# Performance work log

Measured on AMD Instinct MI355X. Metric: run time of the kernel, lower is better.

The kernel has to match this reference:

```python
import math
import jax, jax.numpy as jnp
import numpy as np

H = 1024
NH = 16
HD = H // NH
FF = 4096


def gelu_erf(x):
    return x * 0.5 * (1.0 + jax.lax.erf(x / jnp.sqrt(jnp.float32(2.0))))


def layernorm(x, gamma, beta, eps=1e-12):
    mean = x.mean(axis=-1, keepdims=True)
    var = ((x - mean) ** 2).mean(axis=-1, keepdims=True)
    return gamma * (x - mean) / jnp.sqrt(var + eps) + beta


def setup_inputs() -> dict:
    key = jax.random.key(0)
    ks = jax.random.split(key, 12)
    B, S = 2, 2048
    sc = 0.02
    return {
        "x": jax.random.normal(ks[0], (B, S, H), jnp.float32),
        "attention_mask": jnp.ones((B, S), jnp.int32),
        "Wq": jax.random.normal(ks[1], (H, H), jnp.float32) * sc,
        "bq": jnp.zeros((H,), jnp.float32),
        "Wk": jax.random.normal(ks[2], (H, H), jnp.float32) * sc,
        "bk": jnp.zeros((H,), jnp.float32),
        "Wv": jax.random.normal(ks[3], (H, H), jnp.float32) * sc,
        "bv": jnp.zeros((H,), jnp.float32),
        "Wo": jax.random.normal(ks[4], (H, H), jnp.float32) * sc,
        "bo": jnp.zeros((H,), jnp.float32),
        "ln1_g": jnp.ones((H,), jnp.float32),
        "ln1_b": jnp.zeros((H,), jnp.float32),
        "W1": jax.random.normal(ks[5], (H, FF), jnp.float32) * sc,
        "b1": jnp.zeros((FF,), jnp.float32),
        "W2": jax.random.normal(ks[6], (FF, H), jnp.float32) * sc,
        "b2": jnp.zeros((H,), jnp.float32),
        "ln2_g": jnp.ones((H,), jnp.float32),
        "ln2_b": jnp.zeros((H,), jnp.float32),
    }


def reference(x, attention_mask, Wq, bq, Wk, bk, Wv, bv, Wo, bo,
              ln1_g, ln1_b, W1, b1, W2, b2, ln2_g, ln2_b):
    B, S, _ = x.shape
    # QKV projections, split heads -> [B, NH, S, HD]
    def split(t):
        return t.reshape(B, S, NH, HD).transpose(0, 2, 1, 3)
    q = split(x @ Wq + bq)
    k = split(x @ Wk + bk)
    v = split(x @ Wv + bv)
    # scores [B, NH, S, S]
    s = jnp.einsum("bhqd,bhkd->bhqk", q, k) / math.sqrt(HD)
    mask = (attention_mask == 1)[:, None, None, :]  # [B,1,1,S]
    s = jnp.where(mask, s, -jnp.inf)
    p = jax.nn.softmax(s, axis=-1)
    a = jnp.einsum("bhqk,bhkd->bhqd", p, v)
    a = a.transpose(0, 2, 1, 3).reshape(B, S, H)  # merge heads
    a = a @ Wo + bo
    a = layernorm(a, ln1_g, ln1_b)  # NOTE: no residual in source
    m = gelu_erf(a @ W1 + b1) @ W2 + b2
    return layernorm(m, ln2_g, ln2_b)
```

## Files before the change

### kernel.cpp

```cpp
#include <hip/hip_runtime.h>
#include <hip/hip_bf16.h>
#include <math.h>

typedef __bf16 bf16;
typedef __attribute__((ext_vector_type(8))) __bf16 bf16x8;
typedef __attribute__((ext_vector_type(4))) __bf16 bf16x4;
typedef __attribute__((ext_vector_type(2))) __bf16 bf16x2;
typedef __attribute__((ext_vector_type(4))) float f32x4;
typedef __attribute__((ext_vector_type(4))) short short4v;

#define HDIM 1024
#define NHEAD 16
#define HD 64
#define FFDIM 4096
#define BATCH 2
#define SEQ 2048
#define M_TOK 4096
#define NSPLIT 4
#define PSTRIDE ((size_t)M_TOK * HDIM)

static __device__ __forceinline__ void async_load16(const bf16* g, bf16* l) {
  __builtin_amdgcn_global_load_lds(
      (const __attribute__((address_space(1))) void*)g,
      (__attribute__((address_space(3))) void*)l, 16, 0, 0);
}

static __device__ __forceinline__ f32x4 mfma16_bf16(bf16x4 a, bf16x4 b, f32x4 c) {
#if defined(__HIP_DEVICE_COMPILE__)
#if __has_builtin(__builtin_amdgcn_mfma_f32_16x16x16bf16_1k)
  return __builtin_amdgcn_mfma_f32_16x16x16bf16_1k(
      __builtin_bit_cast(short4v, a), __builtin_bit_cast(short4v, b), c, 0, 0, 0);
#else
  return __builtin_amdgcn_mfma_f32_16x16x16_bf16(a, b, c, 0, 0, 0);
#endif
#else
  return c;
#endif
}

static __device__ __forceinline__ float gelu_erf_f(float x) {
  const float z = x * 0.70710678118f;
  const float az = fabsf(z);
  const float tt = __builtin_amdgcn_rcpf(fmaf(az, 0.3275911f, 1.0f));
  const float poly = tt * fmaf(tt, fmaf(tt, fmaf(tt, fmaf(tt, 1.061405429f,
                     -1.453152027f), 1.421413741f), -0.284496736f), 0.254829592f);
  const float e = __builtin_amdgcn_exp2f(az * az * -1.4426950408889634f);
  float erfv = 1.0f - poly * e;
  erfv = (z < 0.f) ? -erfv : erfv;
  return 0.5f * x * (1.0f + erfv);
}

__global__ __launch_bounds__(256)
void prep_kernel(const float* __restrict__ x,
                 const float* __restrict__ Wq, const float* __restrict__ Wk,
                 const float* __restrict__ Wv, const float* __restrict__ Wo,
                 const float* __restrict__ W1, const float* __restrict__ W2,
                 bf16* __restrict__ Xb, bf16* __restrict__ QKVT,
                 bf16* __restrict__ W1T, bf16* __restrict__ W2T)
{
  const int z = blockIdx.z;
  const int t = threadIdx.x;
  if (z == 12) {
    const size_t base = ((size_t)(blockIdx.y * 32 + blockIdx.x)) * 4096;
#pragma unroll
    for (int j = 0; j < 4; ++j) {
      const size_t i = base + j * 1024 + t * 4;
      f32x4 v = *(const f32x4*)(x + i);
      bf16x4 o;
#pragma unroll
      for (int k = 0; k < 4; ++k) o[k] = (bf16)v[k];
      *(bf16x4*)(Xb + i) = o;
    }
    return;
  }
  const float* ps; bf16* pd; int sld, dld;
  if (z < 4) {
    ps = (z == 0) ? Wq : (z == 1) ? Wk : (z == 2) ? Wv : Wo;
    pd = QKVT + (size_t)z * HDIM * HDIM; sld = 1024; dld = 1024;
  } else if (z < 8) {
    const int c = z - 4;
    ps = W1 + c * 1024; sld = 4096;
    pd = W1T + (size_t)c * 1024 * 1024; dld = 1024;
  } else {
    const int c = z - 8;
    ps = W2 + (size_t)c * 1024 * 1024; sld = 1024;
    pd = W2T + c * 1024; dld = 4096;
  }
  __shared__ float tile[32][33];
  const int tx = t & 31, ty = t >> 5;
  const int c0 = blockIdx.x * 32, r0 = blockIdx.y * 32;
#pragma unroll
  for (int i = 0; i < 32; i += 8)
    tile[ty + i][tx] = ps[(size_t)(r0 + ty + i) * sld + c0 + tx];
  __syncthreads();
  const int rr0 = (t & 15) * 2;
  const int ccb = t >> 4;
#pragma unroll
  for (int i = 0; i < 2; ++i) {
    const int cc = ccb + 16 * i;
    bf16x2 v = {(bf16)tile[rr0][cc], (bf16)tile[rr0 + 1][cc]};
    *(bf16x2*)(pd + (size_t)(c0 + cc) * dld + r0 + rr0) = v;
  }
}

#define BSW(R, C) ((R) * 64 + ((C) ^ (((R) & 7) << 3)))
#define BSW128(R, C) ((R) * 128 + ((C) ^ (((R) & 7) << 3)))

template<int EPI>
__global__ __launch_bounds__(256)
void gemm_bt(const bf16* __restrict__ A, const bf16* __restrict__ Bt,
             const float* __restrict__ b0, const float* __restrict__ b1p,
             const float* __restrict__ b2p, void* __restrict__ Cout,
             int M, int N, int ldk, int kchunk)
{
  __shared__ __align__(16) bf16 Smem[2][128 * 64];
  bf16* As = Smem[0];
  bf16* Bs = Smem[1];
  const int t = threadIdx.x;
  const int wave = t >> 6, lane = t & 63;
  const int lm = lane & 15, qd = lane >> 4;
  const int wm = (wave >> 1) * 64, wn = (wave & 1) * 64;

  const int nwg2d = gridDim.x * gridDim.y;
  const int cpx = nwg2d >> 3;
  const int lin2d = blockIdx.x + gridDim.x * blockIdx.y;
  const int swz = (lin2d & 7) * cpx + (lin2d >> 3);
  const int bxs = swz % gridDim.x;
  const int bys = swz / gridDim.x;
  const int bm = bys * 128, bn = bxs * 128;
  const int kbeg = blockIdx.z * kchunk;

  f32x4 acc[4][4] = {};
  const int srow = t >> 3;
  const int schk = t & 7;

  for (int k0 = kbeg; k0 < kbeg + kchunk; k0 += 64) {
#pragma unroll
    for (int r = 0; r < 4; ++r) {
      const int row = r * 32 + srow;
      const int chunk = schk ^ (row & 7);
      async_load16(A + (size_t)(bm + row) * ldk + (k0 + chunk * 8),
                   (bf16*)((char*)As + r * 4096 + t * 16));
    }
#pragma unroll
    for (int r = 0; r < 4; ++r) {
      const int row = r * 32 + srow;
      const int chunk = schk ^ (row & 7);
      async_load16(Bt + (size_t)(bn + row) * ldk + (k0 + chunk * 8),
                   (bf16*)((char*)Bs + r * 4096 + t * 16));
    }
    __syncthreads();
#pragma unroll
    for (int ks = 0; ks < 2; ++ks) {
      bf16x8 av[4], bv[4];
#pragma unroll
      for (int mt = 0; mt < 4; ++mt) {
        const int row = wm + mt * 16 + lm;
        const int chunk = (ks * 4 + qd) ^ (row & 7);
        av[mt] = *(const bf16x8*)(As + row * 64 + chunk * 8);
      }
#pragma unroll
      for (int nt = 0; nt < 4; ++nt) {
        const int row = wn + nt * 16 + lm;
        const int chunk = (ks * 4 + qd) ^ (row & 7);
        bv[nt] = *(const bf16x8*)(Bs + row * 64 + chunk * 8);
      }
#pragma unroll
      for (int mt = 0; mt < 4; ++mt)
#pragma unroll
        for (int nt = 0; nt < 4; ++nt)
          acc[mt][nt] = __builtin_amdgcn_mfma_f32_16x16x32_bf16(bv[nt], av[mt], acc[mt][nt], 0, 0, 0);
    }
    __syncthreads();
  }

  bf16* tw = &Smem[0][0] + wave * 4096;
  const bool vt = (EPI == 3) && ((bn + wn) >= 2 * HDIM);

#pragma unroll
  for (int nt = 0; nt < 4; ++nt) {
    const int n0 = bn + wn + nt * 16 + qd * 4;
    f32x4 bsv = {0.f, 0.f, 0.f, 0.f};
    if (EPI == 2) bsv = *(const f32x4*)(b0 + n0);
    if (EPI == 3) {
      const int sect = n0 >> 10, c = n0 & 1023;
      const float* bp = (sect == 0) ? b0 : (sect == 1) ? b1p : b2p;
      bsv = *(const f32x4*)(bp + c);
    }
#pragma unroll
    for (int mt = 0; mt < 4; ++mt) {
      f32x4 v;
#pragma unroll
      for (int r = 0; r < 4; ++r) v[r] = acc[mt][nt][r] + bsv[r];
      bf16x4 o;
      if (EPI == 2) {
#pragma unroll
        for (int r = 0; r < 4; ++r) o[r] = (bf16)gelu_erf_f(v[r]);
      } else {
#pragma unroll
        for (int r = 0; r < 4; ++r) o[r] = (bf16)v[r];
      }
      if (!vt) {
        *(bf16x4*)(tw + BSW(mt * 16 + lm, nt * 16 + qd * 4)) = o;
      } else {
#pragma unroll
        for (int r = 0; r < 4; ++r)
          tw[BSW(nt * 16 + qd * 4 + r, mt * 16 + lm)] = o[r];
      }
    }
  }
  const int erow = lane >> 3, ech = lane & 7;
  if (EPI == 1) {
    bf16* dst = (bf16*)Cout + (size_t)blockIdx.z * M * N +
                (size_t)(bm + wm) * N + (bn + wn);
#pragma unroll
    for (int p = 0; p < 8; ++p) {
      const int row = p * 8 + erow;
      bf16x8 val = *(const bf16x8*)(tw + BSW(row, ech * 8));
      *(bf16x8*)(dst + (size_t)row * N + ech * 8) = val;
    }
  } else if (EPI == 2) {
    bf16* dst = (bf16*)Cout + (size_t)(bm + wm) * N + (bn + wn);
#pragma unroll
    for (int p = 0; p < 8; ++p) {
      const int row = p * 8 + erow;
      bf16x8 val = *(const bf16x8*)(tw + BSW(row, ech * 8));
      *(bf16x8*)(dst + (size_t)row * N + ech * 8) = val;
    }
  } else {
    bf16* base = (bf16*)Cout;
    const int sect = (bn + wn) >> 10;
    if (!vt) {
      bf16* dst = base + (size_t)sect * M_TOK * HDIM +
                  (size_t)(bm + wm) * HDIM + ((bn + wn) & 1023);
#pragma unroll
      for (int p = 0; p < 8; ++p) {
        const int row = p * 8 + erow;
        bf16x8 val = *(const bf16x8*)(tw + BSW(row, ech * 8));
        *(bf16x8*)(dst + (size_t)row * HDIM + ech * 8) = val;
      }
    } else {
      const int c0 = (bn + wn) & 1023;
      const int hh = c0 >> 6;
      const int bb = (bm + wm) >> 11, ss0 = (bm + wm) & 2047;
      bf16* dst = base + (size_t)2 * M_TOK * HDIM +
                  (size_t)((bb * NHEAD + hh) * HD) * SEQ + ss0;
#pragma unroll
      for (int p = 0; p < 8; ++p) {
        const int row = p * 8 + erow;
        bf16x8 val = *(const bf16x8*)(tw + BSW(row, ech * 8));
        *(bf16x8*)(dst + (size_t)row * SEQ + ech * 8) = val;
      }
    }
  }
}


#define STAGE_Q(OP, BASEMN, LDSB, KOFF, Q) do { \
    const int rr_ = (Q) * 64 + (t >> 3); \
    const int gc_ = (t & 7) ^ (rr_ & 7); \
    async_load16((OP) + (size_t)((BASEMN) + rr_) * ldk + (KOFF) + gc_ * 8, \
                 (LDSB) + (Q) * 4096 + t * 8); \
  } while (0)

#define STAGE_HALF(OP, BASEMN, LDSB, KOFF, H) do { \
    STAGE_Q(OP, BASEMN, LDSB, KOFF, 2 * (H)); \
    STAGE_Q(OP, BASEMN, LDSB, KOFF, 2 * (H) + 1); \
  } while (0)

#define LOAD_AV(BUF, MH) do { \
    _Pragma("unroll") \
    for (int mt_ = 0; mt_ < 4; ++mt_) { \
      const int row_ = wm + (MH) * 64 + mt_ * 16 + lm; \
      _Pragma("unroll") \
      for (int ks_ = 0; ks_ < 2; ++ks_) { \
        const int c_ = (ks_ * 4 + qd) ^ (row_ & 7); \
        av[mt_][ks_] = *(const bf16x8*)(As_[BUF] + row_ * 64 + c_ * 8); \
      } \
    } \
  } while (0)

#define LOAD_BV(DST, BUF, NH) do { \
    _Pragma("unroll") \
    for (int nt_ = 0; nt_ < 2; ++nt_) { \
      const int row_ = wnb + (NH) * 32 + nt_ * 16 + lm; \
      _Pragma("unroll") \
      for (int ks_ = 0; ks_ < 2; ++ks_) { \
        const int c_ = (ks_ * 4 + qd) ^ (row_ & 7); \
        DST[nt_][ks_] = *(const bf16x8*)(Bs_[BUF] + row_ * 64 + c_ * 8); \
      } \
    } \
  } while (0)

#define MFMA_Q(MH, BV, NH) do { \
    __builtin_amdgcn_s_setprio(1); \
    _Pragma("unroll") \
    for (int mt_ = 0; mt_ < 4; ++mt_) \
      _Pragma("unroll") \
      for (int nt_ = 0; nt_ < 2; ++nt_) \
        _Pragma("unroll") \
        for (int ks_ = 0; ks_ < 2; ++ks_) \
          acc[(MH) * 4 + mt_][(NH) * 2 + nt_] = \
              __builtin_amdgcn_mfma_f32_16x16x32_bf16( \
                  BV[nt_][ks_], av[mt_][ks_], \
                  acc[(MH) * 4 + mt_][(NH) * 2 + nt_], 0, 0, 0); \
    __builtin_amdgcn_s_setprio(0); \
  } while (0)

#define SYNC_PRE() do { \
    __builtin_amdgcn_s_barrier(); \
    asm volatile("s_waitcnt lgkmcnt(0)" ::: "memory"); \
    __builtin_amdgcn_sched_barrier(0); \
  } while (0)
#define SYNC_POST() do { \
    __builtin_amdgcn_s_barrier(); \
    __builtin_amdgcn_sched_barrier(0); \
  } while (0)

#define VMCNT4() asm volatile("s_waitcnt vmcnt(4)" ::: "memory")

#define FOURPH(RB, WAB, KTA, WBB, KTB) do { \
     \
    LOAD_AV(RB, 0); LOAD_BV(bv0, RB, 0); \
    STAGE_HALF(A, bm, As_[WAB], kbeg + (KTA) * 64, 0); \
    SYNC_PRE(); MFMA_Q(0, bv0, 0); SYNC_POST(); \
     \
    LOAD_BV(bv1, RB, 1); \
    STAGE_HALF(A, bm, As_[WAB], kbeg + (KTA) * 64, 1); \
    SYNC_PRE(); MFMA_Q(0, bv1, 1); SYNC_POST(); \
     \
    LOAD_AV(RB, 1); \
    STAGE_HALF(Bt, bn, Bs_[WBB], kbeg + (KTB) * 64, 0); \
    SYNC_PRE(); MFMA_Q(1, bv0, 0); SYNC_POST(); \
     \
    STAGE_HALF(Bt, bn, Bs_[WBB], kbeg + (KTB) * 64, 1); \
    SYNC_PRE(); MFMA_Q(1, bv1, 1); VMCNT4(); SYNC_POST(); \
  } while (0)

template<int EPI>
__global__ __launch_bounds__(512, 2)
void gemm256(const bf16* __restrict__ A, const bf16* __restrict__ Bt,
             const float* __restrict__ b0, const float* __restrict__ b1p,
             const float* __restrict__ b2p, void* __restrict__ Cout,
             int M, int N, int ldk, int kchunk)
{
  __shared__ __align__(16) bf16 SmemAll[4][256 * 64];
  bf16* const As_[2] = {SmemAll[0], SmemAll[1]};
  bf16* const Bs_[2] = {SmemAll[2], SmemAll[3]};

  const int t = threadIdx.x;
  const int wave = t >> 6, lane = t & 63;
  const int lm = lane & 15, qd = lane >> 4;
  const int wm = (wave >> 2) * 128;
  const int wnb = (wave & 3) * 64;

  const int nwg2d = gridDim.x * gridDim.y;
  const int cpx = nwg2d >> 3;
  const int lin2d = blockIdx.x + gridDim.x * blockIdx.y;
  const int swz = (lin2d & 7) * cpx + (lin2d >> 3);
  const int bm = (swz / gridDim.x) * 256, bn = (swz % gridDim.x) * 256;
  const int kbeg = blockIdx.z * kchunk;
  const int NT = kchunk >> 6;

  f32x4 acc[8][4] = {};
  bf16x8 av[4][2], bv0[2][2], bv1[2][2];

  STAGE_HALF(Bt, bn, Bs_[0], kbeg, 0);
  STAGE_HALF(Bt, bn, Bs_[0], kbeg, 1);
  STAGE_HALF(A,  bm, As_[0], kbeg, 0);
  STAGE_HALF(A,  bm, As_[0], kbeg, 1);
  STAGE_HALF(Bt, bn, Bs_[1], kbeg + 64, 0);
  STAGE_HALF(Bt, bn, Bs_[1], kbeg + 64, 1);
  VMCNT4();
  SYNC_POST();

  for (int it = 0; it < NT / 2; ++it) {
    const int tb = 2 * it + 1;
    const int tc = (2 * it + 2) & (NT - 1);
    const int td = (2 * it + 3) & (NT - 1);
    FOURPH(0, 1, tb, 0, tc);
    FOURPH(1, 0, tc, 1, td);
  }

  bf16* tw = &SmemAll[0][0] + wave * 8192;
  const bool vt = (EPI == 3) && ((bn + wnb) >= 2 * HDIM);

#pragma unroll
  for (int nt4 = 0; nt4 < 4; ++nt4) {
    const int n0 = bn + wnb + nt4 * 16 + qd * 4;
    f32x4 bsv = {0.f, 0.f, 0.f, 0.f};
    if (EPI == 2) bsv = *(const f32x4*)(b0 + n0);
    if (EPI == 3) {
      const int sect = n0 >> 10, c = n0 & 1023;
      const float* bp = (sect == 0) ? b0 : (sect == 1) ? b1p : b2p;
      bsv = *(const f32x4*)(bp + c);
    }
#pragma unroll
    for (int mt8 = 0; mt8 < 8; ++mt8) {
      f32x4 v;
#pragma unroll
      for (int r = 0; r < 4; ++r) v[r] = acc[mt8][nt4][r] + bsv[r];
      bf16x4 o;
      if (EPI == 2) {
#pragma unroll
        for (int r = 0; r < 4; ++r) o[r] = (bf16)gelu_erf_f(v[r]);
      } else {
#pragma unroll
        for (int r = 0; r < 4; ++r) o[r] = (bf16)v[r];
      }
      if (!vt) {
        *(bf16x4*)(tw + BSW(mt8 * 16 + lm, nt4 * 16 + qd * 4)) = o;
      } else {
#pragma unroll
        for (int r = 0; r < 4; ++r)
          tw[BSW128(nt4 * 16 + qd * 4 + r, mt8 * 16 + lm)] = o[r];
      }
    }
  }
  const int erow = lane >> 3, ech = lane & 7;
  if (EPI != 3) {
    bf16* dst = (bf16*)Cout +
                ((EPI == 1) ? (size_t)blockIdx.z * M * N : (size_t)0) +
                (size_t)(bm + wm) * N + (bn + wnb);
#pragma unroll
    for (int p = 0; p < 16; ++p) {
      const int row = p * 8 + erow;
      bf16x8 val = *(const bf16x8*)(tw + BSW(row, ech * 8));
      *(bf16x8*)(dst + (size_t)row * N + ech * 8) = val;
    }
  } else {
    bf16* base = (bf16*)Cout;
    const int sect = (bn + wnb) >> 10;
    const int c0 = (bn + wnb) & 1023;
    if (!vt) {
      bf16* dst = base + (size_t)sect * M_TOK * HDIM +
                  (size_t)(bm + wm) * HDIM + c0;
#pragma unroll
      for (int p = 0; p < 16; ++p) {
        const int row = p * 8 + erow;
        bf16x8 val = *(const bf16x8*)(tw + BSW(row, ech * 8));
        *(bf16x8*)(dst + (size_t)row * HDIM + ech * 8) = val;
      }
    } else {
      const int hh = c0 >> 6;
      const int bb = (bm + wm) >> 11, ss0 = (bm + wm) & 2047;
      bf16* dst = base + (size_t)2 * M_TOK * HDIM +
                  (size_t)((bb * NHEAD + hh) * HD) * SEQ + ss0;
#pragma unroll
      for (int p = 0; p < 16; ++p) {
        const int row = p * 4 + qd;
        const int cc = lm * 8;
        bf16x8 val = *(const bf16x8*)(tw + BSW128(row, cc));
        *(bf16x8*)(dst + (size_t)row * SEQ + cc) = val;
      }
    }
  }
}

__global__ __launch_bounds__(256)
void attn_kernel(const bf16* __restrict__ Q, const bf16* __restrict__ Kg,
                 const bf16* __restrict__ Vt, const int* __restrict__ mask,
                 bf16* __restrict__ Po, float* __restrict__ Lp)
{
  __shared__ __align__(16) bf16 Ks[64 * 64];
  __shared__ __align__(16) bf16 Vs[64 * 64];
  __shared__ float madd[64];

  const int t = threadIdx.x;
  const int wave = t >> 6, lane = t & 63;
  const int lm = lane & 15, qd = lane >> 4;

  const int lin = blockIdx.x;
  const int g = (lin & 7) * 16 + (lin >> 7);
  const int qblk = (lin >> 3) & 15;
  const int bh = g >> 2;
  const int split = g & 3;
  const int b = bh >> 4, h = bh & 15;
  const int q0 = qblk * 128 + wave * 32;
  const int kv_beg = split * (SEQ / NSPLIT);

  bf16x8 qf[2][2];
#pragma unroll
  for (int qt = 0; qt < 2; ++qt)
#pragma unroll
    for (int ks = 0; ks < 2; ++ks)
      qf[qt][ks] = *(const bf16x8*)(Q + (size_t)(b * SEQ + q0 + qt * 16 + lm) * HDIM +
                                    h * HD + ks * 32 + qd * 8);

  const bf16 onev = (bf16)1.0f;
  const bf16x4 ones = {onev, onev, onev, onev};
  f32x4 lacc[2] = {};
  f32x4 oacc[2][4] = {};

  const int srow = t >> 3, schk = t & 7;
  const float C = 0.1803368801f;

  for (int kv0 = kv_beg; kv0 < kv_beg + SEQ / NSPLIT; kv0 += 64) {
#pragma unroll
    for (int r = 0; r < 2; ++r) {
      const int row = r * 32 + srow;
      const int g2 = schk ^ (row & 7);
      async_load16(Kg + (size_t)(b * SEQ + kv0 + row) * HDIM + h * HD + g2 * 8,
                   (bf16*)((char*)Ks + r * 4096 + t * 16));
      async_load16(Vt + (size_t)(bh * HD + row) * SEQ + kv0 + g2 * 8,
                   (bf16*)((char*)Vs + r * 4096 + t * 16));
    }
    if (t < 64) madd[t] = (mask[b * SEQ + kv0 + t] == 1) ? 0.f : -1.0e30f;
    __syncthreads();

    bf16x8 kf[2][4];
#pragma unroll
    for (int ks = 0; ks < 2; ++ks)
#pragma unroll
      for (int nt = 0; nt < 4; ++nt) {
        const int row = nt * 16 + lm;
        const int c = (ks * 4 + qd) ^ (row & 7);
        kf[ks][nt] = *(const bf16x8*)(Ks + row * 64 + c * 8);
      }

    bf16x4 pf[2][4];
#pragma unroll
    for (int qt = 0; qt < 2; ++qt) {
      f32x4 sacc[4] = {};
#pragma unroll
      for (int ks = 0; ks < 2; ++ks)
#pragma unroll
        for (int nt = 0; nt < 4; ++nt)
          sacc[nt] = __builtin_amdgcn_mfma_f32_16x16x32_bf16(kf[ks][nt], qf[qt][ks], sacc[nt], 0, 0, 0);
#pragma unroll
      for (int nt = 0; nt < 4; ++nt) {
        f32x4 ma = *(const f32x4*)(madd + nt * 16 + qd * 4);
#pragma unroll
        for (int r = 0; r < 4; ++r)
          pf[qt][nt][r] = (bf16)__builtin_amdgcn_exp2f(fmaf(sacc[nt][r], C, ma[r]));
        lacc[qt] = mfma16_bf16(ones, pf[qt][nt], lacc[qt]);
      }
    }

#pragma unroll
    for (int nt2 = 0; nt2 < 4; ++nt2) {
      const int row = nt2 * 16 + lm;
#pragma unroll
      for (int nt = 0; nt < 4; ++nt) {
        bf16x4 vf = *(const bf16x4*)(Vs + row * 64 +
                     (((nt * 2 + (qd >> 1)) ^ (row & 7)) * 8) + (qd & 1) * 4);
        oacc[0][nt2] = mfma16_bf16(vf, pf[0][nt], oacc[0][nt2]);
        oacc[1][nt2] = mfma16_bf16(vf, pf[1][nt], oacc[1][nt2]);
      }
    }
    __syncthreads();
  }

  bf16* po = Po + (size_t)(split * 32 + bh) * 64 * SEQ;
#pragma unroll
  for (int qt = 0; qt < 2; ++qt) {
#pragma unroll
    for (int nt2 = 0; nt2 < 4; ++nt2)
#pragma unroll
      for (int r = 0; r < 4; ++r)
        po[(size_t)(nt2 * 16 + qd * 4 + r) * SEQ + q0 + qt * 16 + lm] =
            (bf16)oacc[qt][nt2][r];
    if (qd == 0)
      Lp[(size_t)(split * 32 + bh) * SEQ + q0 + qt * 16 + lm] = lacc[qt][0];
  }
}

__global__ __launch_bounds__(256)
void attn_merge(const bf16* __restrict__ Po, const float* __restrict__ Lp,
                bf16* __restrict__ Aout)
{
  __shared__ bf16 tile[64][80];
  __shared__ float linv[64];
  const int t = threadIdx.x;
  const int bh = blockIdx.y;
  const int b = bh >> 4, h = bh & 15;
  const int s0 = blockIdx.x * 64;

  if (t < 64) {
    float l = 0.f;
#pragma unroll
    for (int s = 0; s < NSPLIT; ++s)
      l += Lp[(size_t)(s * 32 + bh) * SEQ + s0 + t];
    linv[t] = 1.0f / l;
  }
  __syncthreads();

#pragma unroll
  for (int it = 0; it < 2; ++it) {
    const int d = (t >> 3) + 32 * it;
    const int sc = (t & 7) * 8;
    float acc[8] = {};
#pragma unroll
    for (int s = 0; s < NSPLIT; ++s) {
      bf16x8 v = *(const bf16x8*)(Po + ((size_t)(s * 32 + bh) * 64 + d) * SEQ + s0 + sc);
#pragma unroll
      for (int j = 0; j < 8; ++j) acc[j] += (float)v[j];
    }
#pragma unroll
    for (int j = 0; j < 8; ++j)
      tile[sc + j][d] = (bf16)(acc[j] * linv[sc + j]);
  }
  __syncthreads();

  const int tok = t >> 2, dc = (t & 3) * 16;
  bf16x8 o0 = *(const bf16x8*)&tile[tok][dc];
  bf16x8 o1 = *(const bf16x8*)&tile[tok][dc + 8];
  bf16* dst = Aout + (size_t)(b * SEQ + s0 + tok) * HDIM + h * HD + dc;
  *(bf16x8*)dst = o0;
  *(bf16x8*)(dst + 8) = o1;
}

template<int NP, int OUT_BF16>
__global__ __launch_bounds__(256)
void ln_sum(const bf16* __restrict__ p, const float* __restrict__ bias,
            const float* __restrict__ gamma, const float* __restrict__ beta,
            void* __restrict__ out)
{
  const int row = blockIdx.x;
  const int t = threadIdx.x;
  f32x4 v = {0.f, 0.f, 0.f, 0.f};
#pragma unroll
  for (int np = 0; np < NP; ++np) {
    bf16x4 u = *(const bf16x4*)(p + np * PSTRIDE + (size_t)row * HDIM + t * 4);
#pragma unroll
    for (int j = 0; j < 4; ++j) v[j] += (float)u[j];
  }
  f32x4 bv0 = *(const f32x4*)(bias + t * 4);
#pragma unroll
  for (int j = 0; j < 4; ++j) v[j] += bv0[j];

  float s = v[0] + v[1] + v[2] + v[3];
  float s2 = v[0] * v[0] + v[1] * v[1] + v[2] * v[2] + v[3] * v[3];
#pragma unroll
  for (int d = 1; d < 64; d <<= 1) { s += __shfl_xor(s, d, 64); s2 += __shfl_xor(s2, d, 64); }
  __shared__ float ss[4], ss2[4];
  const int wave = t >> 6, lane = t & 63;
  if (lane == 0) { ss[wave] = s; ss2[wave] = s2; }
  __syncthreads();
  s = ss[0] + ss[1] + ss[2] + ss[3];
  s2 = ss2[0] + ss2[1] + ss2[2] + ss2[3];
  const float mean = s * (1.0f / HDIM);
  const float var = s2 * (1.0f / HDIM) - mean * mean;
  const float rstd = rsqrtf(var + 1e-12f);
  f32x4 gv = *(const f32x4*)(gamma + t * 4);
  f32x4 bv = *(const f32x4*)(beta + t * 4);
  f32x4 y;
#pragma unroll
  for (int j = 0; j < 4; ++j) y[j] = gv[j] * (v[j] - mean) * rstd + bv[j];
  if (OUT_BF16) {
    bf16x4 o;
#pragma unroll
    for (int j = 0; j < 4; ++j) o[j] = (bf16)y[j];
    *(bf16x4*)((bf16*)out + (size_t)row * HDIM + t * 4) = o;
  } else {
    *(f32x4*)((float*)out + (size_t)row * HDIM + t * 4) = y;
  }
}

extern "C" void kernel_launch(void* const* d_in, const int* in_sizes, int n_in,
                              void* d_out, int out_size, void* d_ws, size_t ws_size,
                              hipStream_t stream)
{
  const float* x    = (const float*)d_in[0];
  const int*   am   = (const int*)d_in[1];
  const float* Wq   = (const float*)d_in[2];
  const float* bq   = (const float*)d_in[3];
  const float* Wk   = (const float*)d_in[4];
  const float* bk   = (const float*)d_in[5];
  const float* Wv   = (const float*)d_in[6];
  const float* bv   = (const float*)d_in[7];
  const float* Wo   = (const float*)d_in[8];
  const float* bo   = (const float*)d_in[9];
  const float* ln1g = (const float*)d_in[10];
  const float* ln1b = (const float*)d_in[11];
  const float* W1   = (const float*)d_in[12];
  const float* b1   = (const float*)d_in[13];
  const float* W2   = (const float*)d_in[14];
  const float* b2   = (const float*)d_in[15];
  const float* ln2g = (const float*)d_in[16];
  const float* ln2b = (const float*)d_in[17];

  char* ws = (char*)d_ws;
  const size_t MB = 1ull << 20;
  bf16*  W1T  = (bf16*)(ws + 0 * MB);
  bf16*  W2T  = (bf16*)(ws + 8 * MB);
  bf16*  Xb   = (bf16*)(ws + 16 * MB);
  bf16*  QKVT = (bf16*)(ws + 24 * MB);
  bf16*  WoT  = QKVT + (size_t)3 * HDIM * HDIM;
  bf16*  Qb   = (bf16*)(ws + 33 * MB);
  bf16*  Kb   = (bf16*)(ws + 41 * MB);
  bf16*  Vtb  = (bf16*)(ws + 49 * MB);
  bf16*  Po   = (bf16*)(ws + 57 * MB);
  float* Lp   = (float*)(ws + 89 * MB);
  bf16*  Ab   = (bf16*)(ws + 16 * MB);
  bf16*  Pw   = (bf16*)(ws + 33 * MB);
  bf16*  L1   = (bf16*)(ws + 65 * MB);
  bf16*  F1   = (bf16*)(ws + 16 * MB);
  bf16*  Pf   = (bf16*)(ws + 48 * MB);

  prep_kernel<<<dim3(32, 32, 13), 256, 0, stream>>>(x, Wq, Wk, Wv, Wo, W1, W2,
                                                    Xb, QKVT, W1T, W2T);

  gemm256<3><<<dim3(3072 / 256, M_TOK / 256, 1), 512, 0, stream>>>(
      Xb, QKVT, bq, bk, bv, Qb, M_TOK, 3072, HDIM, HDIM);

  attn_kernel<<<dim3(2048, 1, 1), 256, 0, stream>>>(Qb, Kb, Vtb, am, Po, Lp);
  attn_merge<<<dim3(SEQ / 64, BATCH * NHEAD), 256, 0, stream>>>(Po, Lp, Ab);

  gemm_bt<1><<<dim3(HDIM / 128, M_TOK / 128, 2), 256, 0, stream>>>(
      Ab, WoT, nullptr, nullptr, nullptr, Pw, M_TOK, HDIM, HDIM, 512);
  ln_sum<2, 1><<<M_TOK, 256, 0, stream>>>(Pw, bo, ln1g, ln1b, L1);

  gemm256<2><<<dim3(FFDIM / 256, M_TOK / 256, 1), 512, 0, stream>>>(
      L1, W1T, b1, nullptr, nullptr, F1, M_TOK, FFDIM, HDIM, HDIM);

  gemm256<1><<<dim3(HDIM / 256, M_TOK / 256, 4), 512, 0, stream>>>(
      F1, W2T, nullptr, nullptr, nullptr, Pf, M_TOK, HDIM, FFDIM, 1024);
  ln_sum<4, 0><<<M_TOK, 256, 0, stream>>>(Pf, b2, ln2g, ln2b, (float*)d_out);
}
```

Before: 328.0 us.

## Double-buffer K/V tiles in attention kernel and precompute mask additive once

The attention kernel now keeps two LDS buffers for the K and V tiles. It issues the async global-to-LDS load for the next tile before computing on the current one, replacing the single-buffer load/sync/compute loop. The per-tile mask conversion is hoisted into a single upfront fill of a 512-entry LDS array. This is meant to hide global load latency behind the MFMA work. The cost is about double the LDS for K/V, which may reduce occupancy, and a vmcnt(0) wait each iteration.

After: 338.9 us. 1.03x slower.

```diff
diff --git a/kernel.cpp b/kernel.cpp
--- a/kernel.cpp
+++ b/kernel.cpp
@@ -318,6 +318,7 @@
   } while (0)
 
 #define VMCNT4() asm volatile("s_waitcnt vmcnt(4)" ::: "memory")
+#define VMCNT0() asm volatile("s_waitcnt vmcnt(0)" ::: "memory")
 
 #define FOURPH(RB, WAB, KTA, WBB, KTB) do { \
      \
@@ -462,9 +463,9 @@
                  const bf16* __restrict__ Vt, const int* __restrict__ mask,
                  bf16* __restrict__ Po, float* __restrict__ Lp)
 {
-  __shared__ __align__(16) bf16 Ks[64 * 64];
-  __shared__ __align__(16) bf16 Vs[64 * 64];
-  __shared__ float madd[64];
+  __shared__ __align__(16) bf16 Ks[2][64 * 64];
+  __shared__ __align__(16) bf16 Vs[2][64 * 64];
+  __shared__ float madd_all[SEQ / NSPLIT];
 
   const int t = threadIdx.x;
   const int wave = t >> 6, lane = t & 63;
@@ -479,6 +480,10 @@
   const int q0 = qblk * 128 + wave * 32;
   const int kv_beg = split * (SEQ / NSPLIT);
 
+#pragma unroll
+  for (int i = 0; i < SEQ / NSPLIT; i += 256)
+    madd_all[i + t] = (mask[b * SEQ + kv_beg + i + t] == 1) ? 0.f : -1.0e30f;
+
   bf16x8 qf[2][2];
 #pragma unroll
   for (int qt = 0; qt < 2; ++qt)
@@ -494,19 +499,33 @@
 
   const int srow = t >> 3, schk = t & 7;
   const float C = 0.1803368801f;
-
-  for (int kv0 = kv_beg; kv0 < kv_beg + SEQ / NSPLIT; kv0 += 64) {
-#pragma unroll
-    for (int r = 0; r < 2; ++r) {
-      const int row = r * 32 + srow;
-      const int g2 = schk ^ (row & 7);
-      async_load16(Kg + (size_t)(b * SEQ + kv0 + row) * HDIM + h * HD + g2 * 8,
-                   (bf16*)((char*)Ks + r * 4096 + t * 16));
-      async_load16(Vt + (size_t)(bh * HD + row) * SEQ + kv0 + g2 * 8,
-                   (bf16*)((char*)Vs + r * 4096 + t * 16));
-    }
-    if (t < 64) madd[t] = (mask[b * SEQ + kv0 + t] == 1) ? 0.f : -1.0e30f;
-    __syncthreads();
+  const int NTILE = SEQ / NSPLIT / 64;
+
+  __syncthreads();
+
+#define ATTN_ISSUE(TILE, NB) do { \
+    const int kv0_ = kv_beg + (TILE) * 64; \
+    _Pragma("unroll") \
+    for (int r_ = 0; r_ < 2; ++r_) { \
+      const int row_ = r_ * 32 + srow; \
+      const int g2_ = schk ^ (row_ & 7); \
+      async_load16(Kg + (size_t)(b * SEQ + kv0_ + row_) * HDIM + h * HD + g2_ * 8, \
+                   (bf16*)((char*)&Ks[NB][0] + r_ * 4096 + t * 16)); \
+      async_load16(Vt + (size_t)(bh * HD + row_) * SEQ + kv0_ + g2_ * 8, \
+                   (bf16*)((char*)&Vs[NB][0] + r_ * 4096 + t * 16)); \
+    } \
+  } while (0)
+
+  ATTN_ISSUE(0, 0);
+
+  for (int tt = 0; tt < NTILE; ++tt) {
+    const int cur = tt & 1;
+    VMCNT0();
+    __builtin_amdgcn_s_barrier();
+    __builtin_amdgcn_sched_barrier(0);
+    if (tt < NTILE - 1) ATTN_ISSUE(tt + 1, cur ^ 1);
+
+    const float* ma_base = madd_all + tt * 64;
 
     bf16x8 kf[2][4];
 #pragma unroll
@@ -515,7 +534,7 @@
       for (int nt = 0; nt < 4; ++nt) {
         const int row = nt * 16 + lm;
         const int c = (ks * 4 + qd) ^ (row & 7);
-        kf[ks][nt] = *(const bf16x8*)(Ks + row * 64 + c * 8);
+        kf[ks][nt] = *(const bf16x8*)(&Ks[cur][0] + row * 64 + c * 8);
       }
 
     bf16x4 pf[2][4];
@@ -529,7 +548,7 @@
           sacc[nt] = __builtin_amdgcn_mfma_f32_16x16x32_bf16(kf[ks][nt], qf[qt][ks], sacc[nt], 0, 0, 0);
 #pragma unroll
       for (int nt = 0; nt < 4; ++nt) {
-        f32x4 ma = *(const f32x4*)(madd + nt * 16 + qd * 4);
+        f32x4 ma = *(const f32x4*)(ma_base + nt * 16 + qd * 4);
 #pragma unroll
         for (int r = 0; r < 4; ++r)
           pf[qt][nt][r] = (bf16)__builtin_amdgcn_exp2f(fmaf(sacc[nt][r], C, ma[r]));
@@ -542,14 +561,14 @@
       const int row = nt2 * 16 + lm;
 #pragma unroll
       for (int nt = 0; nt < 4; ++nt) {
-        bf16x4 vf = *(const bf16x4*)(Vs + row * 64 +
+        bf16x4 vf = *(const bf16x4*)(&Vs[cur][0] + row * 64 +
                      (((nt * 2 + (qd >> 1)) ^ (row & 7)) * 8) + (qd & 1) * 4);
         oacc[0][nt2] = mfma16_bf16(vf, pf[0][nt], oacc[0][nt2]);
         oacc[1][nt2] = mfma16_bf16(vf, pf[1][nt], oacc[1][nt2]);
       }
     }
-    __syncthreads();
-  }
+  }
+#undef ATTN_ISSUE
 
   bf16* po = Po + (size_t)(split * 32 + bh) * 64 * SEQ;
 #pragma unroll
```
